# Optimization experiments

Measured on AMD Instinct MI355X. Metric: run time of the kernel, lower is better.

Reference implementation:

```python
import jax, jax.numpy as jnp
import numpy as np

L, B, D, H, E, K, R = 256, 64, 1024, 16, 8, 2, 64
SCALE_ADAPTER = 0.1


def setup_inputs() -> dict:
    key = jax.random.key(0)
    ks = jax.random.split(key, 10)
    rn = lambda k, shape, s=0.02: jax.random.normal(k, shape, jnp.float32) * s
    return {
        "x": jax.random.normal(ks[0], (L, B, D), jnp.float32),
        "ln1_w": jnp.ones((D,), jnp.float32), "ln1_b": jnp.zeros((D,), jnp.float32),
        "in_proj_w": rn(ks[1], (3 * D, D)), "in_proj_b": jnp.zeros((3 * D,), jnp.float32),
        "out_proj_w": rn(ks[2], (D, D)), "out_proj_b": jnp.zeros((D,), jnp.float32),
        "ln2_w": jnp.ones((D,), jnp.float32), "ln2_b": jnp.zeros((D,), jnp.float32),
        "c_fc_w": rn(ks[3], (4 * D, D)), "c_fc_b": jnp.zeros((4 * D,), jnp.float32),
        "c_proj_w": rn(ks[4], (D, 4 * D)), "c_proj_b": jnp.zeros((D,), jnp.float32),
        "w_gate": rn(ks[5], (D, E), 0.05),
        "down_w": rn(ks[6], (E, R, D)), "down_b": jnp.zeros((E, R), jnp.float32),
        "up_w": rn(ks[7], (E, D, R)), "up_b": jnp.zeros((E, D), jnp.float32),
    }


def _layer_norm(x, w, b, eps=1e-5):
    mu = x.mean(-1, keepdims=True)
    var = ((x - mu) ** 2).mean(-1, keepdims=True)
    return (x - mu) / jnp.sqrt(var + eps) * w + b


def _mha(x, in_w, in_b, out_w, out_b):
    # x: (L,B,D) sequence-first, self-attention q=k=v=x
    hd = D // H
    qkv = x @ in_w.T + in_b                       # (L,B,3D)
    q, k, v = jnp.split(qkv, 3, axis=-1)
    q = q.reshape(L, B, H, hd)
    k = k.reshape(L, B, H, hd)
    v = v.reshape(L, B, H, hd)
    scores = jnp.einsum("lbhd,mbhd->bhlm", q, k) / jnp.sqrt(jnp.float32(hd))
    attn = jax.nn.softmax(scores, axis=-1)
    o = jnp.einsum("bhlm,mbhd->lbhd", attn, v).reshape(L, B, D)
    return o @ out_w.T + out_b


def _cv_squared(t):
    t = t.astype(jnp.float32)
    return t.var(ddof=1) / (t.mean() ** 2 + 1e-10)


def reference(x, ln1_w, ln1_b, in_proj_w, in_proj_b, out_proj_w, out_proj_b,
              ln2_w, ln2_b, c_fc_w, c_fc_b, c_proj_w, c_proj_b,
              w_gate, down_w, down_b, up_w, up_b):
    x = x + _mha(_layer_norm(x, ln1_w, ln1_b), in_proj_w, in_proj_b, out_proj_w, out_proj_b)

    # --- noisy top-k gating (eval path: no noise), routed on token 0 per sequence ---
    logits = x[0] @ w_gate                                    # (B,E)
    top_v, top_i = jax.lax.top_k(logits, min(K + 1, E))
    gk = jax.nn.softmax(top_v[:, :K], axis=1)                 # (B,K)
    gates = jnp.zeros((B, E), jnp.float32).at[jnp.arange(B)[:, None], top_i[:, :K]].set(gk)
    importance = gates.sum(0)
    load = (gates > 0).sum(0)
    moe_loss = (_cv_squared(importance) + _cv_squared(load)) * 0.01

    # --- dense dispatch/combine: y[l,b] = sum_e gates[b,e] * adapter_e(x[l,b]) ---
    h = jax.nn.relu(jnp.einsum("lbd,erd->lber", x, down_w) + down_b)     # (L,B,E,R)
    y = jnp.einsum("lber,edr,be->lbd", h, up_w, gates) + (gates @ up_b)[None]
    y = y * SCALE_ADAPTER

    # --- MLP (QuickGELU) + parallel adapter residual ---
    h2 = _layer_norm(x, ln2_w, ln2_b) @ c_fc_w.T + c_fc_b
    h2 = h2 * jax.nn.sigmoid(1.702 * h2)
    mlp = h2 @ c_proj_w.T + c_proj_b
    x = x + mlp + y
    return x, moe_loss
```

## Files before the change

kernel.cpp:

```cpp
#include <hip/hip_runtime.h>

typedef unsigned short u16;
typedef unsigned int u32;
typedef __bf16 bf16x8 __attribute__((ext_vector_type(8)));
typedef float f32x4 __attribute__((ext_vector_type(4)));

#define MFMA16(a, b, c) __builtin_amdgcn_mfma_f32_16x16x32_bf16(a, b, c, 0, 0, 0)

__device__ __forceinline__ u16 f2bf(float f) {
  u32 u = __builtin_bit_cast(u32, f);
  u32 r = u + 0x7fffu + ((u >> 16) & 1u);
  return (u16)(r >> 16);
}

__device__ __forceinline__ uint4 cvt8(const float4& a, const float4& b) {
  union { u16 h[8]; uint4 q; } u;
  u.h[0] = f2bf(a.x); u.h[1] = f2bf(a.y); u.h[2] = f2bf(a.z); u.h[3] = f2bf(a.w);
  u.h[4] = f2bf(b.x); u.h[5] = f2bf(b.y); u.h[6] = f2bf(b.z); u.h[7] = f2bf(b.w);
  return u.q;
}

__device__ __forceinline__ void gload16(const u16* g, u16* l) {
  __builtin_amdgcn_global_load_lds(
      (const __attribute__((address_space(1))) u32*)g,
      (__attribute__((address_space(3))) u32*)l, 16, 0, 0);
}

template <int MODE>
__global__ __launch_bounds__(512, 2) void gemm256_k(
    const u16* __restrict__ A, int lda,
    const u16* __restrict__ W, int ldb,
    const float* __restrict__ bias, const float* __restrict__ aux0,
    float* __restrict__ outF, u16* __restrict__ outB, int N, int K)
{
  __shared__ u16 As[4][8192];
  __shared__ u16 Bs[4][8192];
  const int tid = threadIdx.x;
  const int nxb = N >> 8;
  const int gsz = nxb << 4;
  const int g = blockIdx.x / gsz;
  const int rem = blockIdx.x - g * gsz;
  const int m0 = ((g << 4) + (rem & 15)) * 256;
  const int n0 = (rem >> 4) * 256;
  const int w = tid >> 6, lane = tid & 63, lr = lane & 15, quad = lane >> 4;
  const int wr = (w >> 2) * 128, wc = (w & 3) * 64;

  f32x4 acc[8][4];
  #pragma unroll
  for (int i = 0; i < 8; i++)
    #pragma unroll
    for (int j = 0; j < 4; j++)
      #pragma unroll
      for (int r = 0; r < 4; r++) acc[i][j][r] = 0.f;

  const int sr = w * 16 + (lane >> 2);
  const int scol = ((lane & 3) ^ ((lane >> 3) & 3)) * 8;
  const u16* gA0 = A + (long)(m0 + sr) * lda + scol;
  const u16* gA1 = gA0 + (long)128 * lda;
  const u16* gB0 = W + (long)(n0 + sr) * ldb + scol;
  const u16* gB1 = gB0 + (long)128 * ldb;
  const int lo = w * 512;
  const int su = (quad ^ ((lr >> 1) & 3)) * 8;

  const int nt = K >> 5;
  #pragma unroll
  for (int p = 0; p < 3; p++) {
    const int kk = p * 32;
    gload16(gA0 + kk, &As[p][lo]);
    gload16(gA1 + kk, &As[p][4096 + lo]);
    gload16(gB0 + kk, &Bs[p][lo]);
    gload16(gB1 + kk, &Bs[p][4096 + lo]);
  }

  for (int t = 0; t < nt; t++) {
    if (t < nt - 2)      asm volatile("s_waitcnt vmcnt(8)" ::: "memory");
    else if (t < nt - 1) asm volatile("s_waitcnt vmcnt(4)" ::: "memory");
    else                 asm volatile("s_waitcnt vmcnt(0)" ::: "memory");
    __builtin_amdgcn_s_barrier();
    asm volatile("" ::: "memory");
    const int tp = t + 3;
    if (tp < nt) {
      const int kn = tp * 32;
      u16* a = As[tp & 3];
      u16* b = Bs[tp & 3];
      gload16(gA0 + kn, a + lo);
      gload16(gA1 + kn, a + 4096 + lo);
      gload16(gB0 + kn, b + lo);
      gload16(gB1 + kn, b + 4096 + lo);
    }
    const u16* Ab = As[t & 3];
    const u16* Bb = Bs[t & 3];
    bf16x8 bfr[4];
    #pragma unroll
    for (int j = 0; j < 4; j++)
      bfr[j] = *(const bf16x8*)&Bb[(wc + j * 16 + lr) * 32 + su];
    __builtin_amdgcn_s_setprio(1);
    #pragma unroll
    for (int i = 0; i < 8; i++) {
      bf16x8 af = *(const bf16x8*)&Ab[(wr + i * 16 + lr) * 32 + su];
      #pragma unroll
      for (int j = 0; j < 4; j++)
        acc[i][j] = MFMA16(af, bfr[j], acc[i][j]);
    }
    __builtin_amdgcn_s_setprio(0);
  }

  #pragma unroll
  for (int i = 0; i < 8; i++) {
    #pragma unroll
    for (int j = 0; j < 4; j++) {
      #pragma unroll
      for (int r = 0; r < 4; r++) {
        const int gm = m0 + wr + i * 16 + quad * 4 + r;
        const int gn = n0 + wc + j * 16 + lr;
        const long oidx = (long)gm * N + gn;
        float v = acc[i][j][r];
        if constexpr (MODE == 0) {
          v += bias[gn];
          outB[oidx] = f2bf(v);
        } else if constexpr (MODE == 1) {
          v += bias[gn] + aux0[oidx];
          outF[oidx] = v;
        } else if constexpr (MODE == 3) {
          outF[oidx] += 0.1f * (v + aux0[(gm & 63) * 1024 + gn]);
        } else if constexpr (MODE == 4) {
          v += bias[gn];
          float e = __expf(-1.702f * v);
          v = v * __builtin_amdgcn_rcpf(1.f + e);
          outB[oidx] = f2bf(v);
        } else {
          if (bias) v += bias[gn];
          outF[oidx] += v;
        }
      }
    }
  }
}

__global__ __launch_bounds__(256) void gemm_down_k(
    const float* __restrict__ Af, int lda,
    const u16* __restrict__ W, int ldb,
    const float* __restrict__ bias, const float* __restrict__ gates,
    u16* __restrict__ outB, int N, int K)
{
  __shared__ u16 As[2][128 * 32];
  __shared__ u16 Bs[2][128 * 32];
  const int tid = threadIdx.x;
  const int nxb = gridDim.x >> 7;
  const int gsz = nxb << 5;
  const int g = blockIdx.x / gsz;
  const int rem = blockIdx.x - g * gsz;
  const int m0 = ((g << 5) + (rem & 31)) * 128;
  const int n0 = (rem >> 5) * 128;
  const int w = tid >> 6, lane = tid & 63, lr = lane & 15, quad = lane >> 4;
  const int wm = (w >> 1) * 64, wn = (w & 1) * 64;

  f32x4 acc[4][4];
  #pragma unroll
  for (int i = 0; i < 4; i++)
    #pragma unroll
    for (int j = 0; j < 4; j++)
      #pragma unroll
      for (int r = 0; r < 4; r++) acc[i][j][r] = 0.f;

  const int srow = w * 32 + (lane >> 2);
  const int scol = (lane & 3) * 8;
  const u16* gB0 = W + (long)(n0 + srow) * ldb + scol;
  const u16* gB1 = gB0 + (long)16 * ldb;
  const int lo = w * 1024;
  const int r0 = tid >> 2, ch0 = (tid & 3) * 8;
  const float* F1 = Af + (long)(m0 + r0) * lda + ch0;
  const float* F2 = Af + (long)(m0 + r0 + 64) * lda + ch0;

  int cur = 0;
  {
    float4 p0 = *(const float4*)(F1);
    float4 p1 = *(const float4*)(F1 + 4);
    float4 q0 = *(const float4*)(F2);
    float4 q1 = *(const float4*)(F2 + 4);
    gload16(gB0, &Bs[0][lo]);
    gload16(gB1, &Bs[0][lo + 512]);
    *(uint4*)&As[0][r0 * 32 + ch0] = cvt8(p0, p1);
    *(uint4*)&As[0][(r0 + 64) * 32 + ch0] = cvt8(q0, q1);
  }
  __syncthreads();
  for (int k0 = 0; k0 < K; k0 += 32) {
    const int kn = k0 + 32;
    const bool more = kn < K;
    float4 p0, p1, q0, q1;
    if (more) {
      p0 = *(const float4*)(F1 + kn);
      p1 = *(const float4*)(F1 + kn + 4);
      q0 = *(const float4*)(F2 + kn);
      q1 = *(const float4*)(F2 + kn + 4);
      gload16(gB0 + kn, &Bs[cur ^ 1][lo]);
      gload16(gB1 + kn, &Bs[cur ^ 1][lo + 512]);
    }
    bf16x8 bfr[4];
    #pragma unroll
    for (int j = 0; j < 4; j++)
      bfr[j] = *(const bf16x8*)&Bs[cur][(wn + j * 16 + lr) * 32 + quad * 8];
    #pragma unroll
    for (int i = 0; i < 4; i++) {
      bf16x8 af = *(const bf16x8*)&As[cur][(wm + i * 16 + lr) * 32 + quad * 8];
      #pragma unroll
      for (int j = 0; j < 4; j++)
        acc[i][j] = MFMA16(af, bfr[j], acc[i][j]);
    }
    if (more) {
      *(uint4*)&As[cur ^ 1][r0 * 32 + ch0] = cvt8(p0, p1);
      *(uint4*)&As[cur ^ 1][(r0 + 64) * 32 + ch0] = cvt8(q0, q1);
    }
    __syncthreads();
    cur ^= 1;
  }

  #pragma unroll
  for (int i = 0; i < 4; i++) {
    #pragma unroll
    for (int j = 0; j < 4; j++) {
      #pragma unroll
      for (int r = 0; r < 4; r++) {
        const int gm = m0 + wm + i * 16 + quad * 4 + r;
        const int gn = n0 + wn + j * 16 + lr;
        float v = acc[i][j][r] + bias[gn];
        v = fmaxf(v, 0.f);
        float g2 = gates[(gm & 63) * 8 + (gn >> 6)];
        outB[(long)gm * N + gn] = f2bf(v * g2);
      }
    }
  }
}

__global__ __launch_bounds__(256) void attn_k(u16* __restrict__ qkv)
{
  __shared__ u16 Vt[64 * 264];
  __shared__ u16 Ps[32 * 264];
  __shared__ float rowstat[64];
  float* red = (float*)Ps;
  const int bh = blockIdx.x, b = bh >> 4, h = bh & 15;
  const int tid = threadIdx.x, w = tid >> 6, lane = tid & 63;
  const int lr = lane & 15, quad = lane >> 4;
  const long base = (long)b * 3072 + h * 64;

  for (int c = tid; c < 2048; c += 256) {
    int m = c >> 3, ch = (c & 7) * 8;
    uint4 vv = *(const uint4*)(qkv + (long)m * 196608 + base + 2048 + ch);
    const u16* s = (const u16*)&vv;
    #pragma unroll
    for (int t = 0; t < 8; t++) Vt[(ch + t) * 264 + m] = s[t];
  }
  __syncthreads();

  for (int qb = 0; qb < 4; qb++) {
    f32x4 acc[4][4];
    #pragma unroll
    for (int i = 0; i < 4; i++)
      #pragma unroll
      for (int j = 0; j < 4; j++)
        #pragma unroll
        for (int r = 0; r < 4; r++) acc[i][j][r] = 0.f;

    #pragma unroll
    for (int ks = 0; ks < 2; ks++) {
      bf16x8 bfr[4];
      #pragma unroll
      for (int j = 0; j < 4; j++) {
        int key = w * 64 + j * 16 + lr;
        bfr[j] = *(const bf16x8*)(qkv + (long)key * 196608 + base + 1024 + ks * 32 + quad * 8);
      }
      #pragma unroll
      for (int i = 0; i < 4; i++) {
        int gq = qb * 64 + i * 16 + lr;
        bf16x8 af = *(const bf16x8*)(qkv + (long)gq * 196608 + base + ks * 32 + quad * 8);
        #pragma unroll
        for (int j = 0; j < 4; j++)
          acc[i][j] = MFMA16(af, bfr[j], acc[i][j]);
      }
    }

    #pragma unroll
    for (int i = 0; i < 4; i++) {
      #pragma unroll
      for (int r = 0; r < 4; r++) {
        float m = -1e30f;
        #pragma unroll
        for (int j = 0; j < 4; j++) {
          float s = acc[i][j][r] * 0.125f;
          acc[i][j][r] = s;
          m = fmaxf(m, s);
        }
        #pragma unroll
        for (int off = 1; off < 16; off <<= 1) m = fmaxf(m, __shfl_xor(m, off));
        if (lr == 0) red[w * 64 + i * 16 + quad * 4 + r] = m;
      }
    }
    __syncthreads();
    if (tid < 64)
      rowstat[tid] = fmaxf(fmaxf(red[tid], red[64 + tid]),
                           fmaxf(red[128 + tid], red[192 + tid]));
    __syncthreads();

    #pragma unroll
    for (int i = 0; i < 4; i++) {
      #pragma unroll
      for (int r = 0; r < 4; r++) {
        float rm = rowstat[i * 16 + quad * 4 + r];
        float s = 0.f;
        #pragma unroll
        for (int j = 0; j < 4; j++) {
          float e = __expf(acc[i][j][r] - rm);
          acc[i][j][r] = e;
          s += e;
        }
        #pragma unroll
        for (int off = 1; off < 16; off <<= 1) s += __shfl_xor(s, off);
        if (lr == 0) red[w * 64 + i * 16 + quad * 4 + r] = s;
      }
    }
    __syncthreads();
    if (tid < 64)
      rowstat[tid] = red[tid] + red[64 + tid] + red[128 + tid] + red[192 + tid];
    __syncthreads();

    #pragma unroll
    for (int hf = 0; hf < 2; hf++) {
      #pragma unroll
      for (int ii = 0; ii < 2; ii++) {
        int i = hf * 2 + ii;
        #pragma unroll
        for (int r = 0; r < 4; r++) {
          int row = i * 16 + quad * 4 + r;
          float inv = 1.f / rowstat[row];
          #pragma unroll
          for (int j = 0; j < 4; j++)
            Ps[(row - hf * 32) * 264 + w * 64 + j * 16 + lr] =
                f2bf(acc[i][j][r] * inv);
        }
      }
      __syncthreads();
      f32x4 o[2];
      #pragma unroll
      for (int j2 = 0; j2 < 2; j2++)
        #pragma unroll
        for (int r = 0; r < 4; r++) o[j2][r] = 0.f;
      #pragma unroll
      for (int ks = 0; ks < 8; ks++) {
        bf16x8 af = *(const bf16x8*)&Ps[((w >> 1) * 16 + lr) * 264 + ks * 32 + quad * 8];
        #pragma unroll
        for (int j2 = 0; j2 < 2; j2++) {
          int j = (w & 1) * 2 + j2;
          bf16x8 bv = *(const bf16x8*)&Vt[(j * 16 + lr) * 264 + ks * 32 + quad * 8];
          o[j2] = MFMA16(af, bv, o[j2]);
        }
      }
      int l0 = qb * 64 + hf * 32 + (w >> 1) * 16 + quad * 4;
      #pragma unroll
      for (int j2 = 0; j2 < 2; j2++) {
        int j = (w & 1) * 2 + j2;
        #pragma unroll
        for (int r = 0; r < 4; r++)
          qkv[(long)(l0 + r) * 196608 + base + j * 16 + lr] = f2bf(o[j2][r]);
      }
      __syncthreads();
    }
  }
}

__global__ __launch_bounds__(256) void ln_k(const float* __restrict__ x,
                                            const float* __restrict__ wt,
                                            const float* __restrict__ bs,
                                            u16* __restrict__ out)
{
  const int tok = blockIdx.x * 4 + (threadIdx.x >> 6);
  const int lane = threadIdx.x & 63;
  const float* xp = x + (long)tok * 1024;
  float4 v[4];
  float s = 0.f, s2 = 0.f;
  #pragma unroll
  for (int t = 0; t < 4; t++) {
    v[t] = *(const float4*)(xp + t * 256 + lane * 4);
    s += v[t].x + v[t].y + v[t].z + v[t].w;
    s2 += v[t].x * v[t].x + v[t].y * v[t].y + v[t].z * v[t].z + v[t].w * v[t].w;
  }
  #pragma unroll
  for (int off = 32; off >= 1; off >>= 1) {
    s += __shfl_xor(s, off);
    s2 += __shfl_xor(s2, off);
  }
  const float m = s * (1.f / 1024.f);
  const float rstd = rsqrtf(s2 * (1.f / 1024.f) - m * m + 1e-5f);
  u16* op = out + (long)tok * 1024;
  #pragma unroll
  for (int t = 0; t < 4; t++) {
    int d = t * 256 + lane * 4;
    float4 wv = *(const float4*)(wt + d);
    float4 bv = *(const float4*)(bs + d);
    union { u16 h[4]; uint2 q; } o;
    o.h[0] = f2bf((v[t].x - m) * rstd * wv.x + bv.x);
    o.h[1] = f2bf((v[t].y - m) * rstd * wv.y + bv.y);
    o.h[2] = f2bf((v[t].z - m) * rstd * wv.z + bv.z);
    o.h[3] = f2bf((v[t].w - m) * rstd * wv.w + bv.w);
    *(uint2*)(op + d) = o.q;
  }
}

__global__ void cvtk(const float* __restrict__ src, u16* __restrict__ dst, int n4)
{
  int i = blockIdx.x * 256 + threadIdx.x;
  if (i >= n4) return;
  float4 v = ((const float4*)src)[i];
  union { u16 h[4]; uint2 q; } o;
  o.h[0] = f2bf(v.x); o.h[1] = f2bf(v.y); o.h[2] = f2bf(v.z); o.h[3] = f2bf(v.w);
  ((uint2*)dst)[i] = o.q;
}

__global__ void wupk(const float* __restrict__ up_w, u16* __restrict__ dst)
{
  int i = blockIdx.x * 256 + threadIdx.x;
  int r = i & 63, e = (i >> 6) & 7, d = i >> 9;
  dst[i] = f2bf(up_w[(e * 1024 + d) * 64 + r]);
}

__global__ __launch_bounds__(256) void gate_k(const float* __restrict__ x1,
                                              const float* __restrict__ wg,
                                              float* __restrict__ gates)
{
  const int wv = threadIdx.x >> 6, lane = threadIdx.x & 63;
  const int b = blockIdx.x * 4 + wv;
  const float* xp = x1 + (long)b * 1024;
  float lg[8];
  #pragma unroll
  for (int e = 0; e < 8; e++) lg[e] = 0.f;
  for (int i = 0; i < 16; i++) {
    int d = i * 64 + lane;
    float xv = xp[d];
    #pragma unroll
    for (int e = 0; e < 8; e++) lg[e] += xv * wg[d * 8 + e];
  }
  #pragma unroll
  for (int e = 0; e < 8; e++)
    #pragma unroll
    for (int off = 32; off >= 1; off >>= 1) lg[e] += __shfl_xor(lg[e], off);
  if (lane == 0) {
    int e1 = 0; float v1 = lg[0];
    #pragma unroll
    for (int e = 1; e < 8; e++) if (lg[e] > v1) { v1 = lg[e]; e1 = e; }
    int e2 = -1; float v2 = -1e30f;
    #pragma unroll
    for (int e = 0; e < 8; e++) if (e != e1 && lg[e] > v2) { v2 = lg[e]; e2 = e; }
    float ex = __expf(v2 - v1);
    float inv = 1.f / (1.f + ex);
    #pragma unroll
    for (int e = 0; e < 8; e++)
      gates[b * 8 + e] = (e == e1) ? inv : ((e == e2) ? ex * inv : 0.f);
  }
}

__global__ void moe_loss_k(const float* __restrict__ gates, float* __restrict__ out)
{
  if (threadIdx.x != 0) return;
  float imp[8], ld[8];
  for (int e = 0; e < 8; e++) { imp[e] = 0.f; ld[e] = 0.f; }
  for (int b = 0; b < 64; b++)
    for (int e = 0; e < 8; e++) {
      float g = gates[b * 8 + e];
      imp[e] += g;
      if (g > 0.f) ld[e] += 1.f;
    }
  float mi = 0.f, ml = 0.f;
  for (int e = 0; e < 8; e++) { mi += imp[e]; ml += ld[e]; }
  mi *= 0.125f; ml *= 0.125f;
  float vi = 0.f, vl = 0.f;
  for (int e = 0; e < 8; e++) {
    float a = imp[e] - mi; vi += a * a;
    float c = ld[e] - ml; vl += c * c;
  }
  vi *= (1.f / 7.f); vl *= (1.f / 7.f);
  out[0] = 0.01f * (vi / (mi * mi + 1e-10f) + vl / (ml * ml + 1e-10f));
}

__global__ __launch_bounds__(256) void gb_k(const float* __restrict__ gates,
                                            const float* __restrict__ up_b,
                                            float* __restrict__ gb)
{
  int b = blockIdx.x, d0 = threadIdx.x * 4;
  float g[8];
  #pragma unroll
  for (int e = 0; e < 8; e++) g[e] = gates[b * 8 + e];
  float s0 = 0, s1 = 0, s2 = 0, s3 = 0;
  #pragma unroll
  for (int e = 0; e < 8; e++) {
    float4 u = *(const float4*)(up_b + e * 1024 + d0);
    s0 += g[e] * u.x; s1 += g[e] * u.y; s2 += g[e] * u.z; s3 += g[e] * u.w;
  }
  float4 r; r.x = s0; r.y = s1; r.z = s2; r.w = s3;
  *(float4*)(gb + b * 1024 + d0) = r;
}

extern "C" void kernel_launch(void* const* d_in, const int* in_sizes, int n_in,
                              void* d_out, int out_size, void* d_ws, size_t ws_size,
                              hipStream_t stream)
{
  (void)in_sizes; (void)n_in; (void)out_size;
  const float* x      = (const float*)d_in[0];
  const float* ln1_w  = (const float*)d_in[1];
  const float* ln1_b  = (const float*)d_in[2];
  const float* in_w   = (const float*)d_in[3];
  const float* in_b   = (const float*)d_in[4];
  const float* out_w  = (const float*)d_in[5];
  const float* out_b  = (const float*)d_in[6];
  const float* ln2_w  = (const float*)d_in[7];
  const float* ln2_b  = (const float*)d_in[8];
  const float* fc_w   = (const float*)d_in[9];
  const float* fc_b   = (const float*)d_in[10];
  const float* pj_w   = (const float*)d_in[11];
  const float* pj_b   = (const float*)d_in[12];
  const float* w_gate = (const float*)d_in[13];
  const float* down_w = (const float*)d_in[14];
  const float* down_b = (const float*)d_in[15];
  const float* up_w   = (const float*)d_in[16];
  const float* up_b   = (const float*)d_in[17];
  float* out = (float*)d_out;
  char* ws = (char*)d_ws;

  u16* wb_in   = (u16*)(ws + 0);
  u16* wb_out  = (u16*)(ws + 6291456);
  u16* wb_down = (u16*)(ws + 8388608);
  u16* wb_up   = (u16*)(ws + 9437184);
  u16* wb_fc   = (u16*)(ws + 0);
  u16* wb_pj   = (u16*)(ws + 10485760);
  float* gates = (float*)(ws + 19005440);
  float* gb    = (float*)(ws + 19007488);
  u16* qkv     = (u16*)(ws + 19269632);
  u16* xln2    = (u16*)(ws + 19269632);
  u16* hg      = (u16*)(ws + 52824064);
  u16* h2      = (u16*)(ws + 69601280);
  u16* xln = (u16*)d_out;

  const bool big = ws_size >= (size_t)203819008;

  cvtk<<<3072, 256, 0, stream>>>(in_w, wb_in, 786432);
  cvtk<<<1024, 256, 0, stream>>>(out_w, wb_out, 262144);
  cvtk<<<512, 256, 0, stream>>>(down_w, wb_down, 131072);
  wupk<<<2048, 256, 0, stream>>>(up_w, wb_up);

  ln_k<<<4096, 256, 0, stream>>>(x, ln1_w, ln1_b, xln);
  gemm256_k<0><<<64 * 12, 512, 0, stream>>>(
      xln, 1024, wb_in, 1024, in_b, nullptr, nullptr, qkv, 3072, 1024);

  attn_k<<<1024, 256, 0, stream>>>(qkv);

  gemm256_k<1><<<64 * 4, 512, 0, stream>>>(
      qkv, 3072, wb_out, 1024, out_b, x, out, nullptr, 1024, 1024);

  gate_k<<<16, 256, 0, stream>>>(out, w_gate, gates);
  moe_loss_k<<<1, 64, 0, stream>>>(gates, out + 16777216);
  gb_k<<<64, 256, 0, stream>>>(gates, up_b, gb);

  ln_k<<<4096, 256, 0, stream>>>(out, ln2_w, ln2_b, xln2);

  gemm_down_k<<<4 * 128, 256, 0, stream>>>(
      out, 1024, wb_down, 1024, down_b, gates, hg, 512, 1024);
  gemm256_k<3><<<64 * 4, 512, 0, stream>>>(
      hg, 512, wb_up, 512, nullptr, gb, out, nullptr, 1024, 512);

  cvtk<<<4096, 256, 0, stream>>>(fc_w, wb_fc, 1048576);
  cvtk<<<4096, 256, 0, stream>>>(pj_w, wb_pj, 1048576);

  if (big) {
    gemm256_k<4><<<64 * 16, 512, 0, stream>>>(
        xln2, 1024, wb_fc, 1024, fc_b, nullptr, nullptr, h2, 4096, 1024);
    gemm256_k<5><<<64 * 4, 512, 0, stream>>>(
        h2, 4096, wb_pj, 4096, pj_b, nullptr, out, nullptr, 1024, 4096);
  } else {
    for (int c = 0; c < 4; c++) {
      gemm256_k<4><<<64 * 4, 512, 0, stream>>>(
          xln2, 1024, wb_fc + (long)c * 1048576, 1024, fc_b + c * 1024,
          nullptr, nullptr, h2, 1024, 1024);
      gemm256_k<5><<<64 * 4, 512, 0, stream>>>(
          h2, 1024, wb_pj + c * 1024, 4096, (c == 0) ? pj_b : nullptr,
          nullptr, out, nullptr, 1024, 1024);
    }
  }
}
```

Before: 1.048 ms.

## Restructure GEMM main loop into ping-pong quadrant schedule with interleaved loads

Replaces the 4-stage ring of 32-wide K tiles with a double-buffered 64-wide K step split into two 32-wide halves. Each half is processed as four 4x2 MFMA quadrants with barriers between them, and the global-to-LDS loads for the next step are interleaved between quadrants. The goal is to overlap LDS fragment reads, global loads and MFMA issue more finely, and to reuse A/B fragments across quadrants to cut register pressure and LDS traffic. In exchange there are many more barriers per iteration and less prefetch depth (two stages instead of four). It also assumes K is a multiple of 64.

```diff
diff --git a/kernel.cpp b/kernel.cpp
--- a/kernel.cpp
+++ b/kernel.cpp
@@ -25,6 +25,10 @@
       (const __attribute__((address_space(1))) u32*)g,
       (__attribute__((address_space(3))) u32*)l, 16, 0, 0);
 }
+
+#define BARF() do { asm volatile("" ::: "memory"); \
+                    __builtin_amdgcn_s_barrier();  \
+                    asm volatile("" ::: "memory"); } while (0)
 
 template <int MODE>
 __global__ __launch_bounds__(512, 2) void gemm256_k(
@@ -33,8 +37,8 @@
     const float* __restrict__ bias, const float* __restrict__ aux0,
     float* __restrict__ outF, u16* __restrict__ outB, int N, int K)
 {
-  __shared__ u16 As[4][8192];
-  __shared__ u16 Bs[4][8192];
+  __shared__ u16 As[2][2][8192];
+  __shared__ u16 Bs[2][2][8192];
   const int tid = threadIdx.x;
   const int nxb = N >> 8;
   const int gsz = nxb << 4;
@@ -59,50 +63,71 @@
   const u16* gA1 = gA0 + (long)128 * lda;
   const u16* gB0 = W + (long)(n0 + sr) * ldb + scol;
   const u16* gB1 = gB0 + (long)128 * ldb;
-  const int lo = w * 512;
+  const int lo = w << 9;
   const int su = (quad ^ ((lr >> 1) & 3)) * 8;
 
-  const int nt = K >> 5;
-  #pragma unroll
-  for (int p = 0; p < 3; p++) {
-    const int kk = p * 32;
-    gload16(gA0 + kk, &As[p][lo]);
-    gload16(gA1 + kk, &As[p][4096 + lo]);
-    gload16(gB0 + kk, &Bs[p][lo]);
-    gload16(gB1 + kk, &Bs[p][4096 + lo]);
-  }
-
-  for (int t = 0; t < nt; t++) {
-    if (t < nt - 2)      asm volatile("s_waitcnt vmcnt(8)" ::: "memory");
-    else if (t < nt - 1) asm volatile("s_waitcnt vmcnt(4)" ::: "memory");
-    else                 asm volatile("s_waitcnt vmcnt(0)" ::: "memory");
-    __builtin_amdgcn_s_barrier();
-    asm volatile("" ::: "memory");
-    const int tp = t + 3;
-    if (tp < nt) {
-      const int kn = tp * 32;
-      u16* a = As[tp & 3];
-      u16* b = Bs[tp & 3];
-      gload16(gA0 + kn, a + lo);
-      gload16(gA1 + kn, a + 4096 + lo);
-      gload16(gB0 + kn, b + lo);
-      gload16(gB1 + kn, b + 4096 + lo);
-    }
-    const u16* Ab = As[t & 3];
-    const u16* Bb = Bs[t & 3];
-    bf16x8 bfr[4];
-    #pragma unroll
-    for (int j = 0; j < 4; j++)
-      bfr[j] = *(const bf16x8*)&Bb[(wc + j * 16 + lr) * 32 + su];
+  auto rdA = [&](bf16x8* af, const u16* tile, int ih) {
+    #pragma unroll
+    for (int i2 = 0; i2 < 4; i2++)
+      af[i2] = *(const bf16x8*)&tile[(wr + ih * 64 + i2 * 16 + lr) * 32 + su];
+  };
+  auto rdB = [&](bf16x8* bfr, const u16* tile, int jh) {
+    #pragma unroll
+    for (int j2 = 0; j2 < 2; j2++)
+      bfr[j2] = *(const bf16x8*)&tile[(wc + jh * 32 + j2 * 16 + lr) * 32 + su];
+  };
+  auto mm8 = [&](int ih, int jh, bf16x8* af, bf16x8* bfr) {
     __builtin_amdgcn_s_setprio(1);
     #pragma unroll
-    for (int i = 0; i < 8; i++) {
-      bf16x8 af = *(const bf16x8*)&Ab[(wr + i * 16 + lr) * 32 + su];
-      #pragma unroll
-      for (int j = 0; j < 4; j++)
-        acc[i][j] = MFMA16(af, bfr[j], acc[i][j]);
-    }
+    for (int i2 = 0; i2 < 4; i2++)
+      #pragma unroll
+      for (int j2 = 0; j2 < 2; j2++)
+        acc[ih * 4 + i2][jh * 2 + j2] =
+            MFMA16(af[i2], bfr[j2], acc[ih * 4 + i2][jh * 2 + j2]);
     __builtin_amdgcn_s_setprio(0);
+  };
+
+  const int nt = K >> 6;
+
+  gload16(gA0,      As[0][0] + lo); gload16(gA1,      As[0][0] + 4096 + lo);
+  gload16(gB0,      Bs[0][0] + lo); gload16(gB1,      Bs[0][0] + 4096 + lo);
+  gload16(gA0 + 32, As[0][1] + lo); gload16(gA1 + 32, As[0][1] + 4096 + lo);
+  gload16(gB0 + 32, Bs[0][1] + lo); gload16(gB1 + 32, Bs[0][1] + 4096 + lo);
+  asm volatile("s_waitcnt vmcnt(0)" ::: "memory");
+  __syncthreads();
+
+  for (int t = 0; t < nt; ++t) {
+    const int cur = t & 1, nb = cur ^ 1;
+    const bool more = (t + 1) < nt;
+    const long kb = (long)(t + 1) * 64;
+    const u16* A0 = As[cur][0]; const u16* A1 = As[cur][1];
+    const u16* B0 = Bs[cur][0]; const u16* B1 = Bs[cur][1];
+    bf16x8 af[4], b0[2], b1[2];
+    rdA(af, A0, 0); rdB(b0, B0, 0);
+    if (more) { gload16(gA0 + kb, As[nb][0] + lo);
+                gload16(gA1 + kb, As[nb][0] + 4096 + lo); }
+    BARF(); mm8(0, 0, af, b0);
+    rdB(b1, B0, 1);
+    BARF(); mm8(0, 1, af, b1);
+    rdA(af, A0, 1);
+    if (more) { gload16(gB0 + kb, Bs[nb][0] + lo);
+                gload16(gB1 + kb, Bs[nb][0] + 4096 + lo); }
+    BARF(); mm8(1, 1, af, b1);
+    if (more) asm volatile("s_waitcnt vmcnt(4)" ::: "memory");
+    else      asm volatile("s_waitcnt vmcnt(0)" ::: "memory");
+    BARF(); mm8(1, 0, af, b0);
+    rdA(af, A1, 0); rdB(b0, B1, 0);
+    if (more) { gload16(gA0 + kb + 32, As[nb][1] + lo);
+                gload16(gA1 + kb + 32, As[nb][1] + 4096 + lo); }
+    BARF(); mm8(0, 0, af, b0);
+    rdB(b1, B1, 1);
+    BARF(); mm8(0, 1, af, b1);
+    rdA(af, A1, 1);
+    if (more) { gload16(gB0 + kb + 32, Bs[nb][1] + lo);
+                gload16(gB1 + kb + 32, Bs[nb][1] + 4096 + lo); }
+    BARF(); mm8(1, 1, af, b1);
+    if (more) asm volatile("s_waitcnt vmcnt(4)" ::: "memory");
+    BARF(); mm8(1, 0, af, b0);
   }
 
   #pragma unroll
```

After: 931.1 us. 1.13x faster.
